# Optimization experiments

Hardware: AMD Instinct MI355X
Metric: run time of the kernel (lower is better)

## Reference

```python
import jax, jax.numpy as jnp
import numpy as np
import math

N = 100000
E = 1600000
D = 256          # input_size
H = 64           # head_size = input_size // n_heads = 256 // 4


def setup_inputs() -> dict:
    key = jax.random.key(0)
    k1, k2, k3, k4, k5 = jax.random.split(key, 5)
    X = jax.random.normal(k1, (N, D), dtype=jnp.float32)
    edge_index = jax.random.randint(k2, (2, E), 0, N, dtype=jnp.int64)
    # Linear(input_size, head_size, bias=False) weights, stored as [D, H] so Q = X @ Wq
    s = 1.0 / math.sqrt(D)
    Wq = jax.random.uniform(k3, (D, H), dtype=jnp.float32, minval=-s, maxval=s)
    Wk = jax.random.uniform(k4, (D, H), dtype=jnp.float32, minval=-s, maxval=s)
    Wv = jax.random.uniform(k5, (D, H), dtype=jnp.float32, minval=-s, maxval=s)
    return {"X": X, "Wq": Wq, "Wk": Wk, "Wv": Wv, "edge_index": edge_index}


def reference(X, Wq, Wk, Wv, edge_index):
    dk = math.sqrt(H)
    Q = X @ Wq  # [N, H]
    K = X @ Wk
    V = X @ Wv
    src = edge_index[0]  # row of sparse matrix -> softmax segment (dim=1 softmax)
    dst = edge_index[1]  # column -> neighbor supplying K/V
    scores = jnp.sum(Q[src] * K[dst], axis=-1) / dk  # [E]
    # per-row (per src node) stable softmax over edges
    m = jax.ops.segment_max(scores, src, num_segments=N)          # [N], -inf for empty rows
    m = jnp.where(jnp.isfinite(m), m, 0.0)
    e = jnp.exp(scores - m[src])                                   # [E]
    denom = jax.ops.segment_sum(e, src, num_segments=N)            # [N]
    alpha = e / jnp.maximum(denom[src], 1e-38)                     # [E]
    # scatter-weighted V aggregation: out[i] = sum_{(i,j) in edges} alpha_ij * V[j]
    out = jax.ops.segment_sum(alpha[:, None] * V[dst], src, num_segments=N)  # [N, H]
    return out
```

## Files before the change

### kernel.cpp

```cpp
#include <hip/hip_runtime.h>

typedef unsigned short u16;
typedef unsigned int u32;
typedef short short8 __attribute__((ext_vector_type(8)));
typedef float f32x4 __attribute__((ext_vector_type(4)));
typedef u32 u32x4 __attribute__((ext_vector_type(4)));

__device__ __forceinline__ u16 f2bf(float f) {
    union { float f; u32 i; } c; c.f = f;
    u32 i = c.i;
    return (u16)((i + 0x7FFFu + ((i >> 16) & 1u)) >> 16);
}
__device__ __forceinline__ float bf2f(u16 u) {
    union { u32 i; float f; } c; c.i = ((u32)u) << 16; return c.f;
}
__device__ __forceinline__ void bf2x(u32 p, float& lo, float& hi) {
    union { u32 i; float f; } a, b;
    a.i = p << 16; b.i = p & 0xFFFF0000u;
    lo = a.f; hi = b.f;
}
__device__ __forceinline__ u32 cvtpk_bf16(float lo, float hi) {
    u32 r;
    asm("v_cvt_pk_bf16_f32 %0, %1, %2" : "=v"(r) : "v"(lo), "v"(hi));
    return r;
}

__global__ void wfrag_kernel(const float* __restrict__ Wq,
                             const float* __restrict__ Wk,
                             const float* __restrict__ Wv,
                             u16* __restrict__ wf)
{
    int idx = blockIdx.x * 256 + threadIdx.x;
    if (idx >= 12 * 8 * 64) return;
    int lane = idx & 63;
    int s = (idx >> 6) & 7;
    int t = idx >> 9;
    int n = t * 16 + (lane & 15);
    const float* Wsrc = (n < 64) ? Wq : ((n < 128) ? Wk : Wv);
    int col = n & 63;
    int kbase = s * 32 + (lane >> 4) * 8;
    u16 o[8];
#pragma unroll
    for (int j = 0; j < 8; ++j) o[j] = f2bf(Wsrc[(size_t)(kbase + j) * 64 + col]);
    *(short8*)(wf + (size_t)idx * 8) = *(const short8*)o;
}

#define TM 32
__global__ __launch_bounds__(256, 2) void qkv_mfma(
    const float* __restrict__ X, const u16* __restrict__ wf,
    float* __restrict__ Qs, u16* __restrict__ KVsb,
    int N, int NT)
{
    __shared__ float xs[TM * 256];

    const int tid  = threadIdx.x;
    const int lane = tid & 63;
    const int wave = tid >> 6;
    const int m    = lane & 15;
    const int quad = lane >> 4;
    const int t0   = wave * 3;

    const short8* wfp = (const short8*)wf;
    short8 bfr0[8], bfr1[8], bfr2[8];
#pragma unroll
    for (int s = 0; s < 8; ++s) {
        bfr0[s] = wfp[(size_t)((t0 + 0) * 8 + s) * 64 + lane];
        bfr1[s] = wfp[(size_t)((t0 + 1) * 8 + s) * 64 + lane];
        bfr2[s] = wfp[(size_t)((t0 + 2) * 8 + s) * 64 + lane];
    }

    for (int tile = blockIdx.x; tile < NT; tile += gridDim.x) {
#pragma unroll
        for (int it = 0; it < 8; ++it) {
            int c0  = (it * 4 + wave) * 64;
            int c   = c0 + lane;
            int row = c >> 6;
            int sblk = (c & 63) ^ (row & 7);
            int arow = tile * TM + row;
            if (arow >= N) arow = N - 1;
            const float* g = X + (size_t)arow * 256 + sblk * 4;
            float* l = xs + c0 * 4;
            __builtin_amdgcn_global_load_lds(
                (const __attribute__((address_space(1))) void*)g,
                (__attribute__((address_space(3))) void*)l, 16, 0, 0);
        }
        __syncthreads();

        f32x4 acc[2][3];
#pragma unroll
        for (int rb = 0; rb < 2; ++rb)
#pragma unroll
            for (int tt = 0; tt < 3; ++tt) acc[rb][tt] = (f32x4)0.f;

#pragma unroll
        for (int rb = 0; rb < 2; ++rb) {
            const int row = rb * 16 + m;
            const float* xrow = xs + row * 256;
            const int sw = m & 7;
#pragma unroll
            for (int s = 0; s < 8; ++s) {
                int B0 = quad * 2 + s * 8;
                float4 a0 = *(const float4*)(xrow + ((B0)     ^ sw) * 4);
                float4 a1 = *(const float4*)(xrow + ((B0 + 1) ^ sw) * 4);
                union { u32x4 u; short8 s8; } af;
                af.u.x = cvtpk_bf16(a0.x, a0.y);
                af.u.y = cvtpk_bf16(a0.z, a0.w);
                af.u.z = cvtpk_bf16(a1.x, a1.y);
                af.u.w = cvtpk_bf16(a1.z, a1.w);
                acc[rb][0] = __builtin_amdgcn_mfma_f32_16x16x32_bf16(af.s8, bfr0[s], acc[rb][0], 0, 0, 0);
                acc[rb][1] = __builtin_amdgcn_mfma_f32_16x16x32_bf16(af.s8, bfr1[s], acc[rb][1], 0, 0, 0);
                acc[rb][2] = __builtin_amdgcn_mfma_f32_16x16x32_bf16(af.s8, bfr2[s], acc[rb][2], 0, 0, 0);
            }
        }

#pragma unroll
        for (int rb = 0; rb < 2; ++rb) {
            int rbase = tile * TM + rb * 16 + quad * 4;
#pragma unroll
            for (int tt = 0; tt < 3; ++tt) {
                int t = t0 + tt;
                int col = (t & 3) * 16 + m;
#pragma unroll
                for (int r = 0; r < 4; ++r) {
                    int rr = rbase + r;
                    if (rr >= N) continue;
                    float v = acc[rb][tt][r];
                    if (t < 4)      Qs  [(size_t)rr * 64  + col]      = v;
                    else if (t < 8) KVsb[(size_t)rr * 128 + col]      = f2bf(v);
                    else            KVsb[(size_t)rr * 128 + 64 + col] = f2bf(v);
                }
            }
        }
        __syncthreads();
    }
}


#define CB 320

__global__ __launch_bounds__(256) void count_kernel(
    const int* __restrict__ src, int* __restrict__ bcnt,
    int E, int N, int NB, int chunk)
{
    __shared__ int cnt[512];
    for (int i = threadIdx.x; i < 512; i += 256) cnt[i] = 0;
    __syncthreads();
    int lo = blockIdx.x * chunk;
    int hi = min(E, lo + chunk);
    for (int e = lo + (int)threadIdx.x; e < hi; e += 256) {
        int s = src[e];
        if ((unsigned)s < (unsigned)N) atomicAdd(&cnt[s >> 8], 1);
    }
    __syncthreads();
    int* row = bcnt + (size_t)blockIdx.x * NB;
    for (int b = threadIdx.x; b < NB; b += 256) row[b] = cnt[b];
}

__global__ __launch_bounds__(512) void scan_kernel(
    const int* __restrict__ bcnt, int* __restrict__ blockbase,
    int* __restrict__ bbase, int* __restrict__ row_ptr_N, int NB)
{
    __shared__ int sd[512];
    int t = threadIdx.x;
    int run = 0;
    if (t < NB) {
        for (int blk = 0; blk < CB; ++blk) {
            int v = bcnt[(size_t)blk * NB + t];
            blockbase[(size_t)blk * NB + t] = run;
            run += v;
        }
    }
    sd[t] = (t < NB) ? run : 0;
    __syncthreads();
    for (int off = 1; off < 512; off <<= 1) {
        int x = (t >= off) ? sd[t - off] : 0;
        __syncthreads();
        sd[t] += x;
        __syncthreads();
    }
    if (t < NB) {
        bbase[t] = sd[t] - run;
        if (t == NB - 1) {
            bbase[NB] = sd[t];
            *row_ptr_N = sd[t];
        }
    }
}

__global__ __launch_bounds__(256) void scatter_pairs_kernel(
    const int* __restrict__ src, const int* __restrict__ dst,
    const int* __restrict__ bbase, const int* __restrict__ blockbase,
    u32* __restrict__ pairs, int E, int N, int NB, int chunk)
{
    __shared__ int cnt[512];
    __shared__ int basei[512];
    for (int i = threadIdx.x; i < 512; i += 256) cnt[i] = 0;
    __syncthreads();
    int lo = blockIdx.x * chunk;
    int hi = min(E, lo + chunk);
    for (int e = lo + (int)threadIdx.x; e < hi; e += 256) {
        int s = src[e];
        if ((unsigned)s < (unsigned)N) atomicAdd(&cnt[s >> 8], 1);
    }
    __syncthreads();
    const int* bb = blockbase + (size_t)blockIdx.x * NB;
    for (int b = threadIdx.x; b < NB; b += 256)
        basei[b] = bbase[b] + bb[b];
    __syncthreads();
    for (int i = threadIdx.x; i < 512; i += 256) cnt[i] = 0;
    __syncthreads();
    for (int e = lo + (int)threadIdx.x; e < hi; e += 256) {
        int s = src[e];
        if ((unsigned)s >= (unsigned)N) continue;
        int d = dst[e];
        if ((unsigned)d >= (unsigned)N) d = 0;
        int bk = s >> 8;
        int p = basei[bk] + atomicAdd(&cnt[bk], 1);
        pairs[p] = (u32)d | ((u32)(s & 255) << 24);
    }
}

#define MAXB 6144
__global__ __launch_bounds__(256) void sort_bucket_kernel(
    const u32* __restrict__ pairs, const int* __restrict__ bbase,
    int* __restrict__ row_ptr, int* __restrict__ sorted_dst, int N)
{
    __shared__ int deg[256];
    __shared__ int off[256];
    __shared__ int cur[256];
    __shared__ int ldst[MAXB];

    int bk = blockIdx.x;
    int n0 = bk * 256;
    int nn = min(256, N - n0);
    int base = bbase[bk];
    int size = bbase[bk + 1] - base;
    int t = threadIdx.x;

    deg[t] = 0;
    __syncthreads();
    for (int i = t; i < size; i += 256)
        atomicAdd(&deg[pairs[base + i] >> 24], 1);
    __syncthreads();
    off[t] = deg[t];
    __syncthreads();
    for (int s = 1; s < 256; s <<= 1) {
        int x = (t >= s) ? off[t - s] : 0;
        __syncthreads();
        off[t] += x;
        __syncthreads();
    }
    int excl = off[t] - deg[t];
    cur[t] = excl;
    if (t < nn) row_ptr[n0 + t] = base + excl;
    __syncthreads();
    int cap = min(size, MAXB);
    for (int i = t; i < size; i += 256) {
        u32 pr = pairs[base + i];
        int p = atomicAdd(&cur[pr >> 24], 1);
        if (p < MAXB) ldst[p] = (int)(pr & 0xFFFFFFu);
    }
    __syncthreads();
    for (int i = t; i < cap; i += 256)
        sorted_dst[base + i] = ldst[i];
    for (int i = cap + t; i < size; i += 256)
        sorted_dst[base + i] = 0;
}

__global__ __launch_bounds__(256) void attn_csr(
    const float* __restrict__ Qs, const u16* __restrict__ KVsb,
    const int* __restrict__ row_ptr, const int* __restrict__ sdst,
    float* __restrict__ out, int N)
{
    int sg = (int)((blockIdx.x * 256 + threadIdx.x) >> 3);
    if (sg >= N) return;
    int sl = threadIdx.x & 7;

    const float* qp = Qs + (size_t)sg * 64 + sl * 8;
    float4 q0 = *(const float4*)(qp);
    float4 q1 = *(const float4*)(qp + 4);

    int beg = row_ptr[sg];
    int end = row_ptr[sg + 1];

    float l = 0.f;
    float a0 = 0.f, a1 = 0.f, a2 = 0.f, a3 = 0.f;
    float a4 = 0.f, a5 = 0.f, a6 = 0.f, a7 = 0.f;

    if (beg < end) {
        const int last = end - 1;
        uint4 kr[8], vr[8];
        int pd[8];

#pragma unroll
        for (int i = 0; i < 8; ++i) {
            int e = beg + i;
            int d = sdst[e <= last ? e : last];
            const u16* kv = KVsb + (size_t)d * 128 + sl * 8;
            kr[i] = *(const uint4*)(kv);
            vr[i] = *(const uint4*)(kv + 64);
            int ep = beg + 8 + i;
            pd[i] = sdst[ep <= last ? ep : last];
        }

        for (int base = beg; base < end; base += 8) {
#pragma unroll
            for (int i = 0; i < 8; ++i) {
                int e = base + i;
                uint4 k = kr[i], v = vr[i];

                {
                    const u16* kv = KVsb + (size_t)pd[i] * 128 + sl * 8;
                    kr[i] = *(const uint4*)(kv);
                    vr[i] = *(const uint4*)(kv + 64);
                    int ep = e + 16;
                    pd[i] = sdst[ep <= last ? ep : last];
                }

                float k0, k1, k2, k3, k4, k5, k6, k7;
                bf2x(k.x, k0, k1); bf2x(k.y, k2, k3);
                bf2x(k.z, k4, k5); bf2x(k.w, k6, k7);

                float p = q0.x * k0 + q0.y * k1 + q0.z * k2 + q0.w * k3
                        + q1.x * k4 + q1.y * k5 + q1.z * k6 + q1.w * k7;
                p += __shfl_xor(p, 1);
                p += __shfl_xor(p, 2);
                p += __shfl_xor(p, 4);

                float pe = __expf(p * 0.125f);

                float v0, v1, v2, v3, v4, v5, v6, v7;
                bf2x(v.x, v0, v1); bf2x(v.y, v2, v3);
                bf2x(v.z, v4, v5); bf2x(v.w, v6, v7);

                if (e < end) {
                    l += pe;
                    a0 += pe * v0; a1 += pe * v1; a2 += pe * v2; a3 += pe * v3;
                    a4 += pe * v4; a5 += pe * v5; a6 += pe * v6; a7 += pe * v7;
                }
            }
        }
    }

    float inv = (l > 0.f) ? (1.f / l) : 0.f;
    float* op = out + (size_t)sg * 64 + sl * 8;
    *(float4*)(op)     = make_float4(a0 * inv, a1 * inv, a2 * inv, a3 * inv);
    *(float4*)(op + 4) = make_float4(a4 * inv, a5 * inv, a6 * inv, a7 * inv);
}

extern "C" void kernel_launch(void* const* d_in, const int* in_sizes, int n_in,
                              void* d_out, int out_size, void* d_ws, size_t ws_size,
                              hipStream_t stream)
{
    const float* X  = (const float*)d_in[0];
    const float* Wq = (const float*)d_in[1];
    const float* Wk = (const float*)d_in[2];
    const float* Wv = (const float*)d_in[3];
    const int*   ei = (const int*)d_in[4];

    const int N = in_sizes[0] / 256;
    const int E = in_sizes[4] / 2;
    const int* src = ei;
    const int* dst = ei + E;
    const int NB = (N + 255) >> 8;

    char* w = (char*)d_ws;
    float* Qs = (float*)w;      w += (size_t)N * 64 * sizeof(float);
    u16* KVsb = (u16*)w;        w += (size_t)N * 128 * sizeof(u16);
    u32* pairs = (u32*)w;       w += (size_t)E * sizeof(u32);
    int* sorted_dst = (int*)w;  w += (size_t)E * sizeof(int);
    int* row_ptr = (int*)w;     w += (size_t)(N + 1) * sizeof(int);
    int* bbase = (int*)w;       w += (size_t)(NB + 1) * sizeof(int);
    int* bcnt = (int*)w;        w += (size_t)CB * NB * sizeof(int);
    int* blockbase = (int*)w;   w += (size_t)CB * NB * sizeof(int);
    u16* wf = (u16*)w;          w += (size_t)12 * 8 * 64 * 8 * sizeof(u16);

    const int chunk = (E + CB - 1) / CB;
    const int NT = (N + TM - 1) / TM;

    wfrag_kernel<<<24, 256, 0, stream>>>(Wq, Wk, Wv, wf);
    qkv_mfma<<<768, 256, 0, stream>>>(X, wf, Qs, KVsb, N, NT);

    count_kernel<<<CB, 256, 0, stream>>>(src, bcnt, E, N, NB, chunk);
    scan_kernel<<<1, 512, 0, stream>>>(bcnt, blockbase, bbase, row_ptr + N, NB);
    scatter_pairs_kernel<<<CB, 256, 0, stream>>>(
        src, dst, bbase, blockbase, pairs, E, N, NB, chunk);
    sort_bucket_kernel<<<NB, 256, 0, stream>>>(pairs, bbase, row_ptr, sorted_dst, N);

    attn_csr<<<(N * 8 + 255) / 256, 256, 0, stream>>>(
        Qs, KVsb, row_ptr, sorted_dst, (float*)d_out, N);
}
```

Before: 324.7 us.

## Fuse edge counting into QKV kernel, fold scan into scatter, shrink attn prefetch

The src-bucket counting blocks are appended to the QKV MFMA launch so they can overlap with the projection. The separate single-block scan kernel is removed: each scatter block recomputes the bucket totals and its own prefix from a transposed count matrix. This drops two launches and the serial scan, at the cost of redundant per-block reduction work. The attention kernel's software prefetch depth is also cut from 8 to 4 edges, which lowers register pressure but hides less gather latency.

```diff
diff --git a/kernel.cpp b/kernel.cpp
--- a/kernel.cpp
+++ b/kernel.cpp
@@ -46,12 +46,33 @@
 }
 
 #define TM 32
-__global__ __launch_bounds__(256, 2) void qkv_mfma(
+#define CB 320
+#define QB 768
+
+__global__ __launch_bounds__(256, 2) void qkv_count(
     const float* __restrict__ X, const u16* __restrict__ wf,
     float* __restrict__ Qs, u16* __restrict__ KVsb,
-    int N, int NT)
+    const int* __restrict__ src, int* __restrict__ bcnt,
+    int N, int NT, int E, int NB, int chunk)
 {
     __shared__ float xs[TM * 256];
+
+    if (blockIdx.x >= QB) {
+        int cb = blockIdx.x - QB;
+        int* cnt = (int*)xs;
+        for (int i = threadIdx.x; i < 512; i += 256) cnt[i] = 0;
+        __syncthreads();
+        int lo = cb * chunk;
+        int hi = min(E, lo + chunk);
+        for (int e = lo + (int)threadIdx.x; e < hi; e += 256) {
+            int s = src[e];
+            if ((unsigned)s < (unsigned)N) atomicAdd(&cnt[s >> 8], 1);
+        }
+        __syncthreads();
+        for (int b = threadIdx.x; b < NB; b += 256)
+            bcnt[(size_t)b * CB + cb] = cnt[b];
+        return;
+    }
 
     const int tid  = threadIdx.x;
     const int lane = tid & 63;
@@ -69,7 +90,7 @@
         bfr2[s] = wfp[(size_t)((t0 + 2) * 8 + s) * 64 + lane];
     }
 
-    for (int tile = blockIdx.x; tile < NT; tile += gridDim.x) {
+    for (int tile = blockIdx.x; tile < NT; tile += QB) {
 #pragma unroll
         for (int it = 0; it < 8; ++it) {
             int c0  = (it * 4 + wave) * 64;
@@ -135,81 +156,64 @@
     }
 }
 
-
-#define CB 320
-
-__global__ __launch_bounds__(256) void count_kernel(
-    const int* __restrict__ src, int* __restrict__ bcnt,
-    int E, int N, int NB, int chunk)
-{
-    __shared__ int cnt[512];
-    for (int i = threadIdx.x; i < 512; i += 256) cnt[i] = 0;
-    __syncthreads();
-    int lo = blockIdx.x * chunk;
-    int hi = min(E, lo + chunk);
-    for (int e = lo + (int)threadIdx.x; e < hi; e += 256) {
-        int s = src[e];
-        if ((unsigned)s < (unsigned)N) atomicAdd(&cnt[s >> 8], 1);
-    }
-    __syncthreads();
-    int* row = bcnt + (size_t)blockIdx.x * NB;
-    for (int b = threadIdx.x; b < NB; b += 256) row[b] = cnt[b];
-}
-
-__global__ __launch_bounds__(512) void scan_kernel(
-    const int* __restrict__ bcnt, int* __restrict__ blockbase,
-    int* __restrict__ bbase, int* __restrict__ row_ptr_N, int NB)
-{
-    __shared__ int sd[512];
-    int t = threadIdx.x;
-    int run = 0;
-    if (t < NB) {
-        for (int blk = 0; blk < CB; ++blk) {
-            int v = bcnt[(size_t)blk * NB + t];
-            blockbase[(size_t)blk * NB + t] = run;
-            run += v;
-        }
-    }
-    sd[t] = (t < NB) ? run : 0;
-    __syncthreads();
-    for (int off = 1; off < 512; off <<= 1) {
-        int x = (t >= off) ? sd[t - off] : 0;
-        __syncthreads();
-        sd[t] += x;
-        __syncthreads();
-    }
-    if (t < NB) {
-        bbase[t] = sd[t] - run;
-        if (t == NB - 1) {
-            bbase[NB] = sd[t];
-            *row_ptr_N = sd[t];
-        }
-    }
-}
-
 __global__ __launch_bounds__(256) void scatter_pairs_kernel(
     const int* __restrict__ src, const int* __restrict__ dst,
-    const int* __restrict__ bbase, const int* __restrict__ blockbase,
-    u32* __restrict__ pairs, int E, int N, int NB, int chunk)
-{
+    const int* __restrict__ bcnt, u32* __restrict__ pairs,
+    int* __restrict__ bbase, int* __restrict__ row_ptr_N,
+    int E, int N, int NB, int chunk)
+{
+    __shared__ int basei[512];
+    __shared__ int sc[512];
     __shared__ int cnt[512];
-    __shared__ int basei[512];
-    for (int i = threadIdx.x; i < 512; i += 256) cnt[i] = 0;
-    __syncthreads();
-    int lo = blockIdx.x * chunk;
+
+    const int blk = blockIdx.x;
+    const int t = threadIdx.x;
+    const int b0 = t, b1 = t + 256;
+
+    int pre0 = 0, tot0 = 0, pre1 = 0, tot1 = 0;
+    if (b0 < NB) {
+        const int* r = bcnt + (size_t)b0 * CB;
+        for (int i = 0; i < CB; ++i) {
+            int v = r[i];
+            tot0 += v;
+            if (i < blk) pre0 += v;
+        }
+    }
+    if (b1 < NB) {
+        const int* r = bcnt + (size_t)b1 * CB;
+        for (int i = 0; i < CB; ++i) {
+            int v = r[i];
+            tot1 += v;
+            if (i < blk) pre1 += v;
+        }
+    }
+    sc[t] = tot0;
+    sc[t + 256] = tot1;
+    __syncthreads();
+    for (int off = 1; off < 512; off <<= 1) {
+        int x0 = (t >= off) ? sc[t - off] : 0;
+        int x1 = sc[t + 256 - off];
+        __syncthreads();
+        sc[t] += x0;
+        sc[t + 256] += x1;
+        __syncthreads();
+    }
+    if (b0 < NB) basei[b0] = (sc[t] - tot0) + pre0;
+    if (b1 < NB) basei[b1] = (sc[t + 256] - tot1) + pre1;
+    if (blk == 0) {
+        if (b0 < NB) bbase[b0] = sc[t] - tot0;
+        if (b1 < NB) bbase[b1] = sc[t + 256] - tot1;
+        if (t == 255) {
+            bbase[NB] = sc[511];
+            *row_ptr_N = sc[511];
+        }
+    }
+    for (int i = t; i < 512; i += 256) cnt[i] = 0;
+    __syncthreads();
+
+    int lo = blk * chunk;
     int hi = min(E, lo + chunk);
-    for (int e = lo + (int)threadIdx.x; e < hi; e += 256) {
-        int s = src[e];
-        if ((unsigned)s < (unsigned)N) atomicAdd(&cnt[s >> 8], 1);
-    }
-    __syncthreads();
-    const int* bb = blockbase + (size_t)blockIdx.x * NB;
-    for (int b = threadIdx.x; b < NB; b += 256)
-        basei[b] = bbase[b] + bb[b];
-    __syncthreads();
-    for (int i = threadIdx.x; i < 512; i += 256) cnt[i] = 0;
-    __syncthreads();
-    for (int e = lo + (int)threadIdx.x; e < hi; e += 256) {
+    for (int e = lo + t; e < hi; e += 256) {
         int s = src[e];
         if ((unsigned)s >= (unsigned)N) continue;
         int d = dst[e];
@@ -289,23 +293,23 @@
 
     if (beg < end) {
         const int last = end - 1;
-        uint4 kr[8], vr[8];
-        int pd[8];
-
-#pragma unroll
-        for (int i = 0; i < 8; ++i) {
+        uint4 kr[4], vr[4];
+        int pd[4];
+
+#pragma unroll
+        for (int i = 0; i < 4; ++i) {
             int e = beg + i;
             int d = sdst[e <= last ? e : last];
             const u16* kv = KVsb + (size_t)d * 128 + sl * 8;
             kr[i] = *(const uint4*)(kv);
             vr[i] = *(const uint4*)(kv + 64);
-            int ep = beg + 8 + i;
+            int ep = beg + 4 + i;
             pd[i] = sdst[ep <= last ? ep : last];
         }
 
-        for (int base = beg; base < end; base += 8) {
-#pragma unroll
-            for (int i = 0; i < 8; ++i) {
+        for (int base = beg; base < end; base += 4) {
+#pragma unroll
+            for (int i = 0; i < 4; ++i) {
                 int e = base + i;
                 uint4 k = kr[i], v = vr[i];
 
@@ -313,7 +317,7 @@
                     const u16* kv = KVsb + (size_t)pd[i] * 128 + sl * 8;
                     kr[i] = *(const uint4*)(kv);
                     vr[i] = *(const uint4*)(kv + 64);
-                    int ep = e + 16;
+                    int ep = e + 8;
                     pd[i] = sdst[ep <= last ? ep : last];
                 }
 
@@ -371,22 +375,19 @@
     int* sorted_dst = (int*)w;  w += (size_t)E * sizeof(int);
     int* row_ptr = (int*)w;     w += (size_t)(N + 1) * sizeof(int);
     int* bbase = (int*)w;       w += (size_t)(NB + 1) * sizeof(int);
-    int* bcnt = (int*)w;        w += (size_t)CB * NB * sizeof(int);
-    int* blockbase = (int*)w;   w += (size_t)CB * NB * sizeof(int);
+    int* bcnt = (int*)w;        w += (size_t)NB * CB * sizeof(int);
     u16* wf = (u16*)w;          w += (size_t)12 * 8 * 64 * 8 * sizeof(u16);
 
     const int chunk = (E + CB - 1) / CB;
     const int NT = (N + TM - 1) / TM;
 
     wfrag_kernel<<<24, 256, 0, stream>>>(Wq, Wk, Wv, wf);
-    qkv_mfma<<<768, 256, 0, stream>>>(X, wf, Qs, KVsb, N, NT);
-
-    count_kernel<<<CB, 256, 0, stream>>>(src, bcnt, E, N, NB, chunk);
-    scan_kernel<<<1, 512, 0, stream>>>(bcnt, blockbase, bbase, row_ptr + N, NB);
+    qkv_count<<<QB + CB, 256, 0, stream>>>(
+        X, wf, Qs, KVsb, src, bcnt, N, NT, E, NB, chunk);
     scatter_pairs_kernel<<<CB, 256, 0, stream>>>(
-        src, dst, bbase, blockbase, pairs, E, N, NB, chunk);
-    sort_bucket_kernel<<<NB, 256, 0, stream>>>(pairs, bbase, row_ptr, sorted_dst, N);
-
+        src, dst, bcnt, pairs, bbase, row_ptr + N, E, N, NB, chunk);
+    sort_bucket_kernel<<<NB, 256, 0, stream>>>(
+        pairs, bbase, row_ptr, sorted_dst, N);
     attn_csr<<<(N * 8 + 255) / 256, 256, 0, stream>>>(
         Qs, KVsb, row_ptr, sorted_dst, (float*)d_out, N);
 }
```

Measured after the change: 312.9 us. 3.6% less time.
